# Optimization experiments

Measured on AMD Instinct MI355X. Metric: run time of the kernel, lower is better.

Reference implementation:

```python
import jax, jax.numpy as jnp
import numpy as np

N_NODES = 500_000
N_EDGES = 16_000_000
N_LAYERS = 49
ALPHA = 0.3  # GCN2Conv alpha; beta = 1.0 (no theta/layer given)

# per-layer activation applied AFTER the conv (layer index 0-based)
_LEAKY = {1, 11, 21, 31, 41}
_SIG = {4, 14, 24, 34, 44}


def setup_inputs() -> dict:
    key = jax.random.key(0)
    k1, k2, k3 = jax.random.split(key, 3)
    x = jax.random.normal(k1, (N_NODES, 1), dtype=jnp.float32)
    adj = jax.random.randint(k2, (2, N_EDGES), 0, N_NODES, dtype=jnp.int64)
    # 49 scalar (1x1) layer weights
    w = jax.random.normal(k3, (N_LAYERS,), dtype=jnp.float32) * 0.1
    return {"input": x, "w": w, "adj": adj}


def _gcn_norm(adj, n):
    # add self-loops, symmetric normalization D^-1/2 (A+I) D^-1/2
    loops = jnp.arange(n, dtype=adj.dtype)
    src = jnp.concatenate([adj[0], loops])
    dst = jnp.concatenate([adj[1], loops])
    deg = jax.ops.segment_sum(jnp.ones(src.shape[0], jnp.float32), dst, num_segments=n)
    dis = 1.0 / jnp.sqrt(deg)  # deg >= 1 due to self-loops
    ew = dis[src] * dis[dst]
    return src, dst, ew


def reference(input, w, adj):
    n = input.shape[0]
    x0 = input.astype(jnp.float32)
    src, dst, ew = _gcn_norm(adj, n)
    ewc = ew[:, None]  # [E+N, 1]

    def gcn2(x, wl):
        h = jax.ops.segment_sum(ewc * x[src], dst, num_segments=n)  # A_hat @ x
        comb = (1.0 - ALPHA) * h + ALPHA * x0                       # residual mix
        return comb * wl                                            # 1x1 weight, beta=1

    x = x0
    for i in range(N_LAYERS):
        y = gcn2(x, w[i])
        if i == 0:
            x = y  # no activation after gcn1
        elif i == N_LAYERS - 1:
            x = n * jax.nn.sigmoid(y)  # CustomSigmoid: len(x) * sigmoid(x)
        elif i in _LEAKY:
            x = jax.nn.leaky_relu(y, 0.01)
        elif i in _SIG:
            x = jax.nn.sigmoid(y)
        else:
            x = jax.nn.relu(y)
        # dropout(p=0.0) is identity
    return jnp.squeeze(x, 1).astype(jnp.int64)
```

## Files before the change

kernel.cpp:

```cpp
#include <hip/hip_runtime.h>
#include <math.h>

#define NN 500000
#define NE 16000000
#define BSH 9
#define NBKT 977
#define PB2 65536
#define NPB2 ((NE + PB2 - 1) / PB2)
#define BKT_CAP 17920

__global__ __launch_bounds__(1024) void hist_kernel(const int4* __restrict__ dst4,
                                                    int* __restrict__ bcnt) {
    __shared__ int lh[NBKT];
    for (int i = threadIdx.x; i < NBKT; i += 1024) lh[i] = 0;
    __syncthreads();
    long base4 = (long)blockIdx.x * (PB2 / 4);
    for (int k = 0; k < PB2 / 4; k += 1024) {
        long i4 = base4 + k + threadIdx.x;
        if (i4 < NE / 4) {
            int4 d = dst4[i4];
            atomicAdd(&lh[d.x >> BSH], 1);
            atomicAdd(&lh[d.y >> BSH], 1);
            atomicAdd(&lh[d.z >> BSH], 1);
            atomicAdd(&lh[d.w >> BSH], 1);
        }
    }
    __syncthreads();
    for (int i = threadIdx.x; i < NBKT; i += 1024) {
        int c = lh[i];
        if (c) atomicAdd(&bcnt[i], c);
    }
}

__global__ __launch_bounds__(256) void scan_buckets(int* __restrict__ bcnt,
                                                    int* __restrict__ bbase) {
    __shared__ int sh[256];
    __shared__ int carry_sh;
    if (threadIdx.x == 0) carry_sh = 0;
    __syncthreads();
    for (int base = 0; base < NBKT; base += 256) {
        int i = base + threadIdx.x;
        int v = (i < NBKT) ? bcnt[i] : 0;
        sh[threadIdx.x] = v;
        __syncthreads();
        for (int off = 1; off < 256; off <<= 1) {
            int t = (threadIdx.x >= off) ? sh[threadIdx.x - off] : 0;
            __syncthreads();
            sh[threadIdx.x] += t;
            __syncthreads();
        }
        int incl = sh[threadIdx.x];
        int c = carry_sh;
        __syncthreads();
        if (i < NBKT) {
            int ex = c + incl - v;
            bbase[i] = ex;
            bcnt[i] = ex;
        }
        if (threadIdx.x == 255) carry_sh = c + incl;
        __syncthreads();
    }
    if (threadIdx.x == 0) bbase[NBKT] = NE;
}

__global__ __launch_bounds__(1024) void partition_kernel(const int4* __restrict__ src4,
                                                         const int4* __restrict__ dst4,
                                                         int* __restrict__ bcur,
                                                         int* __restrict__ ebuf) {
    __shared__ int lh[NBKT];
    for (int i = threadIdx.x; i < NBKT; i += 1024) lh[i] = 0;
    __syncthreads();
    long base4 = (long)blockIdx.x * (PB2 / 4);
    for (int k = 0; k < PB2 / 4; k += 1024) {
        long i4 = base4 + k + threadIdx.x;
        if (i4 < NE / 4) {
            int4 d = dst4[i4];
            atomicAdd(&lh[d.x >> BSH], 1);
            atomicAdd(&lh[d.y >> BSH], 1);
            atomicAdd(&lh[d.z >> BSH], 1);
            atomicAdd(&lh[d.w >> BSH], 1);
        }
    }
    __syncthreads();
    for (int i = threadIdx.x; i < NBKT; i += 1024) {
        int c = lh[i];
        if (c) lh[i] = atomicAdd(&bcur[i], c);
    }
    __syncthreads();
    for (int k = 0; k < PB2 / 4; k += 1024) {
        long i4 = base4 + k + threadIdx.x;
        if (i4 < NE / 4) {
            int4 d = dst4[i4];
            int4 s = src4[i4];
            int pos;
            pos = atomicAdd(&lh[d.x >> BSH], 1); ebuf[pos] = ((d.x & 511) << 19) | s.x;
            pos = atomicAdd(&lh[d.y >> BSH], 1); ebuf[pos] = ((d.y & 511) << 19) | s.y;
            pos = atomicAdd(&lh[d.z >> BSH], 1); ebuf[pos] = ((d.z & 511) << 19) | s.z;
            pos = atomicAdd(&lh[d.w >> BSH], 1); ebuf[pos] = ((d.w & 511) << 19) | s.w;
        }
    }
}

__global__ __launch_bounds__(512) void bucket_csr(const int* __restrict__ bbase,
                                                  int* __restrict__ ebuf,
                                                  int* __restrict__ rp,
                                                  float* __restrict__ dis,
                                                  const float* __restrict__ x0,
                                                  float* __restrict__ z0) {
    __shared__ int eds[BKT_CAP];
    __shared__ int outb[BKT_CAP];
    __shared__ int cnt[512];
    __shared__ int scn[512];
    int b = blockIdx.x;
    int ebase = bbase[b];
    int nb = bbase[b + 1] - ebase;
    if (nb > BKT_CAP) nb = BKT_CAP;
    for (int i = threadIdx.x; i < nb; i += 512) eds[i] = ebuf[ebase + i];
    cnt[threadIdx.x] = 0;
    __syncthreads();
    for (int i = threadIdx.x; i < nb; i += 512) atomicAdd(&cnt[eds[i] >> 19], 1);
    __syncthreads();
    int my = cnt[threadIdx.x];
    scn[threadIdx.x] = my;
    __syncthreads();
    for (int off = 1; off < 512; off <<= 1) {
        int t = (threadIdx.x >= off) ? scn[threadIdx.x - off] : 0;
        __syncthreads();
        scn[threadIdx.x] += t;
        __syncthreads();
    }
    int excl = scn[threadIdx.x] - my;
    int v = b * 512 + threadIdx.x;
    if (v < NN) {
        rp[v] = ebase + excl;
        float dv = rsqrtf((float)(my + 1));
        dis[v] = dv;
        z0[v] = x0[v] * dv;
    }
    __syncthreads();
    cnt[threadIdx.x] = excl;
    __syncthreads();
    for (int i = threadIdx.x; i < nb; i += 512) {
        int p = eds[i];
        int pos = atomicAdd(&cnt[p >> 19], 1);
        outb[pos] = p & 0x7FFFF;
    }
    __syncthreads();
    for (int i = threadIdx.x; i < nb; i += 512) ebuf[ebase + i] = outb[i];
    if (b == 0 && threadIdx.x == 0) rp[NN] = NE;
}

__global__ __launch_bounds__(256) void layer_kernel(
        const int* __restrict__ rp, const int* __restrict__ csr,
        const float* __restrict__ zin, const float* __restrict__ dis,
        const float* __restrict__ x0, const float* __restrict__ w,
        int li, int act, float* __restrict__ zout, int* __restrict__ out) {
    int tid = blockIdx.x * 256 + threadIdx.x;
    int v = tid >> 3;
    int lane = threadIdx.x & 7;
    int beg = rp[v];
    int end = rp[v + 1];
    float s = 0.f;
    int j = beg + lane;
    for (; j + 24 < end; j += 32) {
        int c0 = csr[j];
        int c1 = csr[j + 8];
        int c2 = csr[j + 16];
        int c3 = csr[j + 24];
        float z0 = __hip_atomic_load(&zin[c0], __ATOMIC_RELAXED, __HIP_MEMORY_SCOPE_AGENT);
        float z1 = __hip_atomic_load(&zin[c1], __ATOMIC_RELAXED, __HIP_MEMORY_SCOPE_AGENT);
        float z2 = __hip_atomic_load(&zin[c2], __ATOMIC_RELAXED, __HIP_MEMORY_SCOPE_AGENT);
        float z3 = __hip_atomic_load(&zin[c3], __ATOMIC_RELAXED, __HIP_MEMORY_SCOPE_AGENT);
        s += z0; s += z1; s += z2; s += z3;
    }
    for (; j < end; j += 8)
        s += __hip_atomic_load(&zin[csr[j]], __ATOMIC_RELAXED, __HIP_MEMORY_SCOPE_AGENT);
    s += __shfl_xor(s, 1);
    s += __shfl_xor(s, 2);
    s += __shfl_xor(s, 4);
    if (lane != 0) return;
    s += zin[v];
    float h = dis[v] * s;
    float comb = 0.7f * h + 0.3f * x0[v];
    float y = comb * w[li];
    if (act == 4) {
        float sg = 1.f / (1.f + expf(-y));
        out[v] = (int)(500000.f * sg);
        return;
    }
    float r;
    if (act == 0)      r = y;
    else if (act == 1) r = fmaxf(y, 0.f);
    else if (act == 2) r = (y > 0.f) ? y : 0.01f * y;
    else               r = 1.f / (1.f + expf(-y));
    zout[v] = dis[v] * r;
}

extern "C" void kernel_launch(void* const* d_in, const int* in_sizes, int n_in,
                              void* d_out, int out_size, void* d_ws, size_t ws_size,
                              hipStream_t stream) {
    const float* x0  = (const float*)d_in[0];
    const float* w   = (const float*)d_in[1];
    const int*   adj = (const int*)d_in[2];
    const int*   src = adj;
    const int*   dst = adj + NE;
    int* out = (int*)d_out;

    uintptr_t p = (uintptr_t)d_ws;
    auto alloc = [&](size_t bytes) -> void* {
        p = (p + 255) & ~(uintptr_t)255;
        void* r = (void*)p;
        p += bytes;
        return r;
    };
    float* dis   = (float*)alloc((size_t)NN * 4);
    int*   rp    = (int*)alloc((size_t)(NN + 1) * 4);
    float* z0    = (float*)alloc((size_t)NN * 4);
    float* z1    = (float*)alloc((size_t)NN * 4);
    int*   bcnt  = (int*)alloc((size_t)NBKT * 4);
    int*   bbase = (int*)alloc((size_t)(NBKT + 1) * 4);
    int*   csr   = (int*)alloc((size_t)NE * 4);
    (void)ws_size;

    hipMemsetAsync(bcnt, 0, (size_t)NBKT * 4, stream);

    hist_kernel<<<NPB2, 1024, 0, stream>>>((const int4*)dst, bcnt);
    scan_buckets<<<1, 256, 0, stream>>>(bcnt, bbase);
    partition_kernel<<<NPB2, 1024, 0, stream>>>((const int4*)src, (const int4*)dst, bcnt, csr);
    bucket_csr<<<NBKT, 512, 0, stream>>>(bbase, csr, rp, dis, x0, z0);

    float* zbuf[2] = {z0, z1};
    const int LB = (NN * 8) / 256;
    for (int i = 0; i < 49; i++) {
        int act;
        if (i == 0)            act = 0;
        else if (i == 48)      act = 4;
        else if (i % 10 == 1)  act = 2;
        else if (i % 10 == 4)  act = 3;
        else                   act = 1;
        layer_kernel<<<LB, 256, 0, stream>>>(rp, csr, zbuf[i & 1], dis, x0, w,
                                             i, act, zbuf[(i + 1) & 1], out);
    }
}
```

Baseline: 4.054 ms.

## Replace CSR pull SpMV with 2D-tiled shared-memory scatter and combine pass

```diff
diff --git a/kernel.cpp b/kernel.cpp
--- a/kernel.cpp
+++ b/kernel.cpp
@@ -1,199 +1,244 @@
 #include <hip/hip_runtime.h>
 #include <math.h>
+#include <stdint.h>
 
 #define NN 500000
 #define NE 16000000
-#define BSH 9
-#define NBKT 977
-#define PB2 65536
-#define NPB2 ((NE + PB2 - 1) / PB2)
-#define BKT_CAP 17920
-
-__global__ __launch_bounds__(1024) void hist_kernel(const int4* __restrict__ dst4,
+#define NT 62
+#define NQ 8
+#define OCTW 62500
+#define NCH (NT * NQ)
+#define PB 65536
+#define NPB ((NE + PB - 1) / PB)
+#define CH_CAP 34000
+#define ZPAD 524288
+#define SENT 0xFFFFFFFFu
+
+__global__ __launch_bounds__(1024) void hist_kernel(const int4* __restrict__ src4,
+                                                    const int4* __restrict__ dst4,
                                                     int* __restrict__ bcnt) {
-    __shared__ int lh[NBKT];
-    for (int i = threadIdx.x; i < NBKT; i += 1024) lh[i] = 0;
-    __syncthreads();
-    long base4 = (long)blockIdx.x * (PB2 / 4);
-    for (int k = 0; k < PB2 / 4; k += 1024) {
+    __shared__ int lh[NCH];
+    for (int i = threadIdx.x; i < NCH; i += 1024) lh[i] = 0;
+    __syncthreads();
+    long base4 = (long)blockIdx.x * (PB / 4);
+    for (int k = 0; k < PB / 4; k += 1024) {
         long i4 = base4 + k + threadIdx.x;
         if (i4 < NE / 4) {
             int4 d = dst4[i4];
-            atomicAdd(&lh[d.x >> BSH], 1);
-            atomicAdd(&lh[d.y >> BSH], 1);
-            atomicAdd(&lh[d.z >> BSH], 1);
-            atomicAdd(&lh[d.w >> BSH], 1);
+            int4 s = src4[i4];
+            atomicAdd(&lh[(d.x >> 13) * NQ + s.x / OCTW], 1);
+            atomicAdd(&lh[(d.y >> 13) * NQ + s.y / OCTW], 1);
+            atomicAdd(&lh[(d.z >> 13) * NQ + s.z / OCTW], 1);
+            atomicAdd(&lh[(d.w >> 13) * NQ + s.w / OCTW], 1);
         }
     }
     __syncthreads();
-    for (int i = threadIdx.x; i < NBKT; i += 1024) {
+    for (int i = threadIdx.x; i < NCH; i += 1024) {
         int c = lh[i];
         if (c) atomicAdd(&bcnt[i], c);
     }
 }
 
-__global__ __launch_bounds__(256) void scan_buckets(int* __restrict__ bcnt,
-                                                    int* __restrict__ bbase) {
-    __shared__ int sh[256];
-    __shared__ int carry_sh;
-    if (threadIdx.x == 0) carry_sh = 0;
-    __syncthreads();
-    for (int base = 0; base < NBKT; base += 256) {
-        int i = base + threadIdx.x;
-        int v = (i < NBKT) ? bcnt[i] : 0;
-        sh[threadIdx.x] = v;
-        __syncthreads();
-        for (int off = 1; off < 256; off <<= 1) {
-            int t = (threadIdx.x >= off) ? sh[threadIdx.x - off] : 0;
-            __syncthreads();
-            sh[threadIdx.x] += t;
-            __syncthreads();
-        }
-        int incl = sh[threadIdx.x];
-        int c = carry_sh;
-        __syncthreads();
-        if (i < NBKT) {
-            int ex = c + incl - v;
-            bbase[i] = ex;
-            bcnt[i] = ex;
-        }
-        if (threadIdx.x == 255) carry_sh = c + incl;
-        __syncthreads();
-    }
-    if (threadIdx.x == 0) bbase[NBKT] = NE;
+__global__ __launch_bounds__(512) void scan_buckets(const int* __restrict__ bcnt,
+                                                    int* __restrict__ bbase,
+                                                    int* __restrict__ bcur) {
+    __shared__ int scn[512];
+    __shared__ int tot;
+    int i = threadIdx.x;
+    int v = (i < NCH) ? bcnt[i] : 0;
+    int pv = (v + 15) & ~15;
+    scn[i] = pv;
+    __syncthreads();
+    for (int off = 1; off < 512; off <<= 1) {
+        int t = (i >= off) ? scn[i - off] : 0;
+        __syncthreads();
+        scn[i] += t;
+        __syncthreads();
+    }
+    int excl = scn[i] - pv;
+    if (i < NCH) { bbase[i] = excl; bcur[i] = excl; }
+    if (i == 511) tot = scn[511];
+    __syncthreads();
+    if (i == 0) bbase[NCH] = tot;
 }
 
 __global__ __launch_bounds__(1024) void partition_kernel(const int4* __restrict__ src4,
                                                          const int4* __restrict__ dst4,
                                                          int* __restrict__ bcur,
-                                                         int* __restrict__ ebuf) {
-    __shared__ int lh[NBKT];
-    for (int i = threadIdx.x; i < NBKT; i += 1024) lh[i] = 0;
-    __syncthreads();
-    long base4 = (long)blockIdx.x * (PB2 / 4);
-    for (int k = 0; k < PB2 / 4; k += 1024) {
+                                                         uint32_t* __restrict__ ebuf) {
+    __shared__ int lh[NCH];
+    for (int i = threadIdx.x; i < NCH; i += 1024) lh[i] = 0;
+    __syncthreads();
+    long base4 = (long)blockIdx.x * (PB / 4);
+    for (int k = 0; k < PB / 4; k += 1024) {
         long i4 = base4 + k + threadIdx.x;
         if (i4 < NE / 4) {
             int4 d = dst4[i4];
-            atomicAdd(&lh[d.x >> BSH], 1);
-            atomicAdd(&lh[d.y >> BSH], 1);
-            atomicAdd(&lh[d.z >> BSH], 1);
-            atomicAdd(&lh[d.w >> BSH], 1);
+            int4 s = src4[i4];
+            atomicAdd(&lh[(d.x >> 13) * NQ + s.x / OCTW], 1);
+            atomicAdd(&lh[(d.y >> 13) * NQ + s.y / OCTW], 1);
+            atomicAdd(&lh[(d.z >> 13) * NQ + s.z / OCTW], 1);
+            atomicAdd(&lh[(d.w >> 13) * NQ + s.w / OCTW], 1);
         }
     }
     __syncthreads();
-    for (int i = threadIdx.x; i < NBKT; i += 1024) {
+    for (int i = threadIdx.x; i < NCH; i += 1024) {
         int c = lh[i];
         if (c) lh[i] = atomicAdd(&bcur[i], c);
     }
     __syncthreads();
-    for (int k = 0; k < PB2 / 4; k += 1024) {
+    for (int k = 0; k < PB / 4; k += 1024) {
         long i4 = base4 + k + threadIdx.x;
         if (i4 < NE / 4) {
             int4 d = dst4[i4];
             int4 s = src4[i4];
             int pos;
-            pos = atomicAdd(&lh[d.x >> BSH], 1); ebuf[pos] = ((d.x & 511) << 19) | s.x;
-            pos = atomicAdd(&lh[d.y >> BSH], 1); ebuf[pos] = ((d.y & 511) << 19) | s.y;
-            pos = atomicAdd(&lh[d.z >> BSH], 1); ebuf[pos] = ((d.z & 511) << 19) | s.z;
-            pos = atomicAdd(&lh[d.w >> BSH], 1); ebuf[pos] = ((d.w & 511) << 19) | s.w;
+            pos = atomicAdd(&lh[(d.x >> 13) * NQ + s.x / OCTW], 1);
+            ebuf[pos] = ((uint32_t)(d.x & 8191) << 19) | (uint32_t)s.x;
+            pos = atomicAdd(&lh[(d.y >> 13) * NQ + s.y / OCTW], 1);
+            ebuf[pos] = ((uint32_t)(d.y & 8191) << 19) | (uint32_t)s.y;
+            pos = atomicAdd(&lh[(d.z >> 13) * NQ + s.z / OCTW], 1);
+            ebuf[pos] = ((uint32_t)(d.z & 8191) << 19) | (uint32_t)s.z;
+            pos = atomicAdd(&lh[(d.w >> 13) * NQ + s.w / OCTW], 1);
+            ebuf[pos] = ((uint32_t)(d.w & 8191) << 19) | (uint32_t)s.w;
         }
     }
 }
 
-__global__ __launch_bounds__(512) void bucket_csr(const int* __restrict__ bbase,
-                                                  int* __restrict__ ebuf,
-                                                  int* __restrict__ rp,
-                                                  float* __restrict__ dis,
-                                                  const float* __restrict__ x0,
-                                                  float* __restrict__ z0) {
-    __shared__ int eds[BKT_CAP];
-    __shared__ int outb[BKT_CAP];
-    __shared__ int cnt[512];
-    __shared__ int scn[512];
-    int b = blockIdx.x;
-    int ebase = bbase[b];
-    int nb = bbase[b + 1] - ebase;
-    if (nb > BKT_CAP) nb = BKT_CAP;
-    for (int i = threadIdx.x; i < nb; i += 512) eds[i] = ebuf[ebase + i];
-    cnt[threadIdx.x] = 0;
-    __syncthreads();
-    for (int i = threadIdx.x; i < nb; i += 512) atomicAdd(&cnt[eds[i] >> 19], 1);
-    __syncthreads();
-    int my = cnt[threadIdx.x];
-    scn[threadIdx.x] = my;
-    __syncthreads();
-    for (int off = 1; off < 512; off <<= 1) {
-        int t = (threadIdx.x >= off) ? scn[threadIdx.x - off] : 0;
-        __syncthreads();
-        scn[threadIdx.x] += t;
-        __syncthreads();
-    }
-    int excl = scn[threadIdx.x] - my;
-    int v = b * 512 + threadIdx.x;
+__global__ __launch_bounds__(1024) void chunk_sort(const int* __restrict__ bcnt,
+                                                   const int* __restrict__ bbase,
+                                                   uint32_t* __restrict__ ebuf,
+                                                   int* __restrict__ deg) {
+    __shared__ uint32_t sorted[CH_CAP];
+    __shared__ int ghist[4096];
+    __shared__ int scn[1024];
+    int c = blockIdx.x;
+    int base = bbase[c];
+    int pend = bbase[c + 1];
+    int n = bcnt[c];
+    if (n > CH_CAP) n = CH_CAP;
+    int t = c >> 3;
+    int octbase = (c & 7) * OCTW;
+    int* dh = (int*)sorted;
+    for (int i = threadIdx.x; i < 4096; i += 1024) ghist[i] = 0;
+    for (int i = threadIdx.x; i < 8192; i += 1024) dh[i] = 0;
+    __syncthreads();
+    for (int i = threadIdx.x; i < n; i += 1024) {
+        uint32_t w = ebuf[base + i];
+        int s = (int)(w & 0x7FFFFu);
+        atomicAdd(&ghist[(s - octbase) >> 4], 1);
+        atomicAdd(&dh[w >> 19], 1);
+    }
+    __syncthreads();
+    for (int i = threadIdx.x; i < 8192; i += 1024) {
+        int d = dh[i];
+        if (d) atomicAdd(&deg[t * 8192 + i], d);
+    }
+    __syncthreads();
+    int b4 = threadIdx.x * 4;
+    int l0 = ghist[b4], l1 = ghist[b4 + 1], l2 = ghist[b4 + 2], l3 = ghist[b4 + 3];
+    int ls = l0 + l1 + l2 + l3;
+    scn[threadIdx.x] = ls;
+    __syncthreads();
+    for (int off = 1; off < 1024; off <<= 1) {
+        int tv = (threadIdx.x >= off) ? scn[threadIdx.x - off] : 0;
+        __syncthreads();
+        scn[threadIdx.x] += tv;
+        __syncthreads();
+    }
+    int ex = scn[threadIdx.x] - ls;
+    ghist[b4] = ex; ghist[b4 + 1] = ex + l0;
+    ghist[b4 + 2] = ex + l0 + l1; ghist[b4 + 3] = ex + l0 + l1 + l2;
+    __syncthreads();
+    for (int i = threadIdx.x; i < n; i += 1024) {
+        uint32_t w = ebuf[base + i];
+        int k = ((int)(w & 0x7FFFFu) - octbase) >> 4;
+        int pos = atomicAdd(&ghist[k], 1);
+        sorted[pos] = w;
+    }
+    __syncthreads();
+    for (int i = threadIdx.x; base + i < pend; i += 1024)
+        ebuf[base + i] = (i < n) ? sorted[i] : SENT;
+}
+
+__global__ void dis_kernel(const int* __restrict__ deg, const float* __restrict__ x0,
+                           float* __restrict__ dis, float* __restrict__ z0) {
+    int v = blockIdx.x * 512 + threadIdx.x;
     if (v < NN) {
-        rp[v] = ebase + excl;
-        float dv = rsqrtf((float)(my + 1));
-        dis[v] = dv;
-        z0[v] = x0[v] * dv;
-    }
-    __syncthreads();
-    cnt[threadIdx.x] = excl;
-    __syncthreads();
-    for (int i = threadIdx.x; i < nb; i += 512) {
-        int p = eds[i];
-        int pos = atomicAdd(&cnt[p >> 19], 1);
-        outb[pos] = p & 0x7FFFF;
-    }
-    __syncthreads();
-    for (int i = threadIdx.x; i < nb; i += 512) ebuf[ebase + i] = outb[i];
-    if (b == 0 && threadIdx.x == 0) rp[NN] = NE;
-}
-
-__global__ __launch_bounds__(256) void layer_kernel(
-        const int* __restrict__ rp, const int* __restrict__ csr,
-        const float* __restrict__ zin, const float* __restrict__ dis,
-        const float* __restrict__ x0, const float* __restrict__ w,
-        int li, int act, float* __restrict__ zout, int* __restrict__ out) {
-    int tid = blockIdx.x * 256 + threadIdx.x;
-    int v = tid >> 3;
-    int lane = threadIdx.x & 7;
-    int beg = rp[v];
-    int end = rp[v + 1];
-    float s = 0.f;
-    int j = beg + lane;
-    for (; j + 24 < end; j += 32) {
-        int c0 = csr[j];
-        int c1 = csr[j + 8];
-        int c2 = csr[j + 16];
-        int c3 = csr[j + 24];
-        float z0 = __hip_atomic_load(&zin[c0], __ATOMIC_RELAXED, __HIP_MEMORY_SCOPE_AGENT);
-        float z1 = __hip_atomic_load(&zin[c1], __ATOMIC_RELAXED, __HIP_MEMORY_SCOPE_AGENT);
-        float z2 = __hip_atomic_load(&zin[c2], __ATOMIC_RELAXED, __HIP_MEMORY_SCOPE_AGENT);
-        float z3 = __hip_atomic_load(&zin[c3], __ATOMIC_RELAXED, __HIP_MEMORY_SCOPE_AGENT);
-        s += z0; s += z1; s += z2; s += z3;
-    }
-    for (; j < end; j += 8)
-        s += __hip_atomic_load(&zin[csr[j]], __ATOMIC_RELAXED, __HIP_MEMORY_SCOPE_AGENT);
-    s += __shfl_xor(s, 1);
-    s += __shfl_xor(s, 2);
-    s += __shfl_xor(s, 4);
-    if (lane != 0) return;
-    s += zin[v];
-    float h = dis[v] * s;
-    float comb = 0.7f * h + 0.3f * x0[v];
-    float y = comb * w[li];
+        float d = rsqrtf((float)(deg[v] + 1));
+        dis[v] = d;
+        z0[v] = x0[v] * d;
+    }
+}
+
+__global__ __launch_bounds__(1024) void scatter_kernel(const int* __restrict__ bbase,
+                                                       const uint32_t* __restrict__ ebuf,
+                                                       const float* __restrict__ zin,
+                                                       float* __restrict__ hp) {
+    __shared__ float acc[8192];
+    int c = blockIdx.x;
+    for (int i = threadIdx.x; i < 8192; i += 1024) acc[i] = 0.f;
+    __syncthreads();
+    int b4 = bbase[c] >> 2, e4 = bbase[c + 1] >> 2;
+    const uint4* __restrict__ eb4 = (const uint4*)ebuf;
+    for (int i4 = b4 + threadIdx.x; i4 < e4; i4 += 1024) {
+        uint4 w = eb4[i4];
+        float a0 = zin[w.x & 0x7FFFFu];
+        float a1 = zin[w.y & 0x7FFFFu];
+        float a2 = zin[w.z & 0x7FFFFu];
+        float a3 = zin[w.w & 0x7FFFFu];
+        atomicAdd(&acc[w.x >> 19], a0);
+        atomicAdd(&acc[w.y >> 19], a1);
+        atomicAdd(&acc[w.z >> 19], a2);
+        atomicAdd(&acc[w.w >> 19], a3);
+    }
+    __syncthreads();
+    int t = c >> 3, q = c & 7;
+    float* dstp = hp + (size_t)q * (NT * 8192) + t * 8192;
+    for (int k = threadIdx.x; k < 8192; k += 1024) dstp[k] = acc[k];
+}
+
+__global__ __launch_bounds__(512) void combine_kernel(const float4* __restrict__ hp4,
+        const float4* __restrict__ zin4, const float4* __restrict__ dis4,
+        const float4* __restrict__ x04, const float* __restrict__ w,
+        int li, int act, float4* __restrict__ zout4, int4* __restrict__ out4) {
+    int v4 = blockIdx.x * 512 + threadIdx.x;
+    if (v4 >= NN / 4) return;
+    float4 s = zin4[v4];
+    #pragma unroll
+    for (int q = 0; q < NQ; q++) {
+        float4 hq = hp4[(size_t)q * (NT * 8192 / 4) + v4];
+        s.x += hq.x; s.y += hq.y; s.z += hq.z; s.w += hq.w;
+    }
+    float4 dv = dis4[v4];
+    float4 xv = x04[v4];
+    float wl = w[li];
+    float y0 = (0.7f * dv.x * s.x + 0.3f * xv.x) * wl;
+    float y1 = (0.7f * dv.y * s.y + 0.3f * xv.y) * wl;
+    float y2 = (0.7f * dv.z * s.z + 0.3f * xv.z) * wl;
+    float y3 = (0.7f * dv.w * s.w + 0.3f * xv.w) * wl;
     if (act == 4) {
-        float sg = 1.f / (1.f + expf(-y));
-        out[v] = (int)(500000.f * sg);
+        int4 o;
+        o.x = (int)(500000.f / (1.f + expf(-y0)));
+        o.y = (int)(500000.f / (1.f + expf(-y1)));
+        o.z = (int)(500000.f / (1.f + expf(-y2)));
+        o.w = (int)(500000.f / (1.f + expf(-y3)));
+        out4[v4] = o;
         return;
     }
-    float r;
-    if (act == 0)      r = y;
-    else if (act == 1) r = fmaxf(y, 0.f);
-    else if (act == 2) r = (y > 0.f) ? y : 0.01f * y;
-    else               r = 1.f / (1.f + expf(-y));
-    zout[v] = dis[v] * r;
+    float r0, r1, r2, r3;
+    if (act == 0)      { r0 = y0; r1 = y1; r2 = y2; r3 = y3; }
+    else if (act == 1) { r0 = fmaxf(y0, 0.f); r1 = fmaxf(y1, 0.f);
+                         r2 = fmaxf(y2, 0.f); r3 = fmaxf(y3, 0.f); }
+    else if (act == 2) { r0 = (y0 > 0.f) ? y0 : 0.01f * y0;
+                         r1 = (y1 > 0.f) ? y1 : 0.01f * y1;
+                         r2 = (y2 > 0.f) ? y2 : 0.01f * y2;
+                         r3 = (y3 > 0.f) ? y3 : 0.01f * y3; }
+    else               { r0 = 1.f / (1.f + expf(-y0)); r1 = 1.f / (1.f + expf(-y1));
+                         r2 = 1.f / (1.f + expf(-y2)); r3 = 1.f / (1.f + expf(-y3)); }
+    float4 zo;
+    zo.x = dv.x * r0; zo.y = dv.y * r1; zo.z = dv.z * r2; zo.w = dv.w * r3;
+    zout4[v4] = zo;
 }
 
 extern "C" void kernel_launch(void* const* d_in, const int* in_sizes, int n_in,
@@ -214,23 +259,29 @@
         return r;
     };
     float* dis   = (float*)alloc((size_t)NN * 4);
-    int*   rp    = (int*)alloc((size_t)(NN + 1) * 4);
-    float* z0    = (float*)alloc((size_t)NN * 4);
-    float* z1    = (float*)alloc((size_t)NN * 4);
-    int*   bcnt  = (int*)alloc((size_t)NBKT * 4);
-    int*   bbase = (int*)alloc((size_t)(NBKT + 1) * 4);
-    int*   csr   = (int*)alloc((size_t)NE * 4);
+    float* z0    = (float*)alloc((size_t)ZPAD * 4);
+    float* z1    = (float*)alloc((size_t)ZPAD * 4);
+    int*   bcnt  = (int*)alloc((size_t)NCH * 4);
+    int*   bbase = (int*)alloc((size_t)(NCH + 1) * 4);
+    int*   bcur  = (int*)alloc((size_t)NCH * 4);
+    uint32_t* csr = (uint32_t*)alloc(((size_t)NE + 8192) * 4);
+    float* hp    = (float*)alloc((size_t)NQ * NT * 8192 * 4);
+    int*   deg   = (int*)hp;
     (void)ws_size;
 
-    hipMemsetAsync(bcnt, 0, (size_t)NBKT * 4, stream);
-
-    hist_kernel<<<NPB2, 1024, 0, stream>>>((const int4*)dst, bcnt);
-    scan_buckets<<<1, 256, 0, stream>>>(bcnt, bbase);
-    partition_kernel<<<NPB2, 1024, 0, stream>>>((const int4*)src, (const int4*)dst, bcnt, csr);
-    bucket_csr<<<NBKT, 512, 0, stream>>>(bbase, csr, rp, dis, x0, z0);
+    hipMemsetAsync(bcnt, 0, (size_t)NCH * 4, stream);
+    hipMemsetAsync(deg, 0, (size_t)NT * 8192 * 4, stream);
+    hipMemsetAsync(z0, 0, (size_t)ZPAD * 4, stream);
+    hipMemsetAsync(z1, 0, (size_t)ZPAD * 4, stream);
+
+    hist_kernel<<<NPB, 1024, 0, stream>>>((const int4*)src, (const int4*)dst, bcnt);
+    scan_buckets<<<1, 512, 0, stream>>>(bcnt, bbase, bcur);
+    partition_kernel<<<NPB, 1024, 0, stream>>>((const int4*)src, (const int4*)dst, bcur, csr);
+    chunk_sort<<<NCH, 1024, 0, stream>>>(bcnt, bbase, csr, deg);
+    dis_kernel<<<(NN + 511) / 512, 512, 0, stream>>>(deg, x0, dis, z0);
 
     float* zbuf[2] = {z0, z1};
-    const int LB = (NN * 8) / 256;
+    const int CB = (NN / 4 + 511) / 512;
     for (int i = 0; i < 49; i++) {
         int act;
         if (i == 0)            act = 0;
@@ -238,7 +289,9 @@
         else if (i % 10 == 1)  act = 2;
         else if (i % 10 == 4)  act = 3;
         else                   act = 1;
-        layer_kernel<<<LB, 256, 0, stream>>>(rp, csr, zbuf[i & 1], dis, x0, w,
-                                             i, act, zbuf[(i + 1) & 1], out);
-    }
-}
+        scatter_kernel<<<NCH, 1024, 0, stream>>>(bbase, csr, zbuf[i & 1], hp);
+        combine_kernel<<<CB, 512, 0, stream>>>((const float4*)hp, (const float4*)zbuf[i & 1],
+                                               (const float4*)dis, (const float4*)x0, w,
+                                               i, act, (float4*)zbuf[(i + 1) & 1], (int4*)out);
+    }
+}
```

Measured after the change: 4.935 ms. 21.7% more time.

## Partition edges into fixed-capacity bucket slots and use nontemporal CSR loads

Applied to the files above, without the earlier changes.

```diff
diff --git a/kernel.cpp b/kernel.cpp
--- a/kernel.cpp
+++ b/kernel.cpp
@@ -3,107 +3,58 @@
 
 #define NN 500000
 #define NE 16000000
-#define BSH 9
 #define NBKT 977
-#define PB2 65536
-#define NPB2 ((NE + PB2 - 1) / PB2)
+#define PB 65536
+#define NPB ((NE + PB - 1) / PB)
 #define BKT_CAP 17920
+#define SLOTB 17920
 
-__global__ __launch_bounds__(1024) void hist_kernel(const int4* __restrict__ dst4,
-                                                    int* __restrict__ bcnt) {
+__global__ __launch_bounds__(1024) void partition_kernel(const int4* __restrict__ src4,
+                                                         const int4* __restrict__ dst4,
+                                                         int* __restrict__ bcnt,
+                                                         int* __restrict__ ebuf) {
     __shared__ int lh[NBKT];
     for (int i = threadIdx.x; i < NBKT; i += 1024) lh[i] = 0;
     __syncthreads();
-    long base4 = (long)blockIdx.x * (PB2 / 4);
-    for (int k = 0; k < PB2 / 4; k += 1024) {
+    long base4 = (long)blockIdx.x * (PB / 4);
+    for (int k = 0; k < PB / 4; k += 1024) {
         long i4 = base4 + k + threadIdx.x;
         if (i4 < NE / 4) {
             int4 d = dst4[i4];
-            atomicAdd(&lh[d.x >> BSH], 1);
-            atomicAdd(&lh[d.y >> BSH], 1);
-            atomicAdd(&lh[d.z >> BSH], 1);
-            atomicAdd(&lh[d.w >> BSH], 1);
+            atomicAdd(&lh[d.x >> 9], 1);
+            atomicAdd(&lh[d.y >> 9], 1);
+            atomicAdd(&lh[d.z >> 9], 1);
+            atomicAdd(&lh[d.w >> 9], 1);
         }
     }
     __syncthreads();
     for (int i = threadIdx.x; i < NBKT; i += 1024) {
         int c = lh[i];
-        if (c) atomicAdd(&bcnt[i], c);
-    }
-}
-
-__global__ __launch_bounds__(256) void scan_buckets(int* __restrict__ bcnt,
-                                                    int* __restrict__ bbase) {
-    __shared__ int sh[256];
-    __shared__ int carry_sh;
-    if (threadIdx.x == 0) carry_sh = 0;
-    __syncthreads();
-    for (int base = 0; base < NBKT; base += 256) {
-        int i = base + threadIdx.x;
-        int v = (i < NBKT) ? bcnt[i] : 0;
-        sh[threadIdx.x] = v;
-        __syncthreads();
-        for (int off = 1; off < 256; off <<= 1) {
-            int t = (threadIdx.x >= off) ? sh[threadIdx.x - off] : 0;
-            __syncthreads();
-            sh[threadIdx.x] += t;
-            __syncthreads();
-        }
-        int incl = sh[threadIdx.x];
-        int c = carry_sh;
-        __syncthreads();
-        if (i < NBKT) {
-            int ex = c + incl - v;
-            bbase[i] = ex;
-            bcnt[i] = ex;
-        }
-        if (threadIdx.x == 255) carry_sh = c + incl;
-        __syncthreads();
-    }
-    if (threadIdx.x == 0) bbase[NBKT] = NE;
-}
-
-__global__ __launch_bounds__(1024) void partition_kernel(const int4* __restrict__ src4,
-                                                         const int4* __restrict__ dst4,
-                                                         int* __restrict__ bcur,
-                                                         int* __restrict__ ebuf) {
-    __shared__ int lh[NBKT];
-    for (int i = threadIdx.x; i < NBKT; i += 1024) lh[i] = 0;
-    __syncthreads();
-    long base4 = (long)blockIdx.x * (PB2 / 4);
-    for (int k = 0; k < PB2 / 4; k += 1024) {
-        long i4 = base4 + k + threadIdx.x;
-        if (i4 < NE / 4) {
-            int4 d = dst4[i4];
-            atomicAdd(&lh[d.x >> BSH], 1);
-            atomicAdd(&lh[d.y >> BSH], 1);
-            atomicAdd(&lh[d.z >> BSH], 1);
-            atomicAdd(&lh[d.w >> BSH], 1);
-        }
+        if (c) lh[i] = atomicAdd(&bcnt[i], c);
     }
     __syncthreads();
-    for (int i = threadIdx.x; i < NBKT; i += 1024) {
-        int c = lh[i];
-        if (c) lh[i] = atomicAdd(&bcur[i], c);
-    }
-    __syncthreads();
-    for (int k = 0; k < PB2 / 4; k += 1024) {
+    for (int k = 0; k < PB / 4; k += 1024) {
         long i4 = base4 + k + threadIdx.x;
         if (i4 < NE / 4) {
             int4 d = dst4[i4];
             int4 s = src4[i4];
-            int pos;
-            pos = atomicAdd(&lh[d.x >> BSH], 1); ebuf[pos] = ((d.x & 511) << 19) | s.x;
-            pos = atomicAdd(&lh[d.y >> BSH], 1); ebuf[pos] = ((d.y & 511) << 19) | s.y;
-            pos = atomicAdd(&lh[d.z >> BSH], 1); ebuf[pos] = ((d.z & 511) << 19) | s.z;
-            pos = atomicAdd(&lh[d.w >> BSH], 1); ebuf[pos] = ((d.w & 511) << 19) | s.w;
+            int b, rel;
+            b = d.x >> 9; rel = atomicAdd(&lh[b], 1);
+            if (rel < SLOTB) ebuf[(long)b * SLOTB + rel] = ((d.x & 511) << 19) | s.x;
+            b = d.y >> 9; rel = atomicAdd(&lh[b], 1);
+            if (rel < SLOTB) ebuf[(long)b * SLOTB + rel] = ((d.y & 511) << 19) | s.y;
+            b = d.z >> 9; rel = atomicAdd(&lh[b], 1);
+            if (rel < SLOTB) ebuf[(long)b * SLOTB + rel] = ((d.z & 511) << 19) | s.z;
+            b = d.w >> 9; rel = atomicAdd(&lh[b], 1);
+            if (rel < SLOTB) ebuf[(long)b * SLOTB + rel] = ((d.w & 511) << 19) | s.w;
         }
     }
 }
 
-__global__ __launch_bounds__(512) void bucket_csr(const int* __restrict__ bbase,
+__global__ __launch_bounds__(512) void bucket_csr(const int* __restrict__ bcnt,
                                                   int* __restrict__ ebuf,
                                                   int* __restrict__ rp,
+                                                  int* __restrict__ re,
                                                   float* __restrict__ dis,
                                                   const float* __restrict__ x0,
                                                   float* __restrict__ z0) {
@@ -112,8 +63,8 @@
     __shared__ int cnt[512];
     __shared__ int scn[512];
     int b = blockIdx.x;
-    int ebase = bbase[b];
-    int nb = bbase[b + 1] - ebase;
+    long ebase = (long)b * SLOTB;
+    int nb = bcnt[b];
     if (nb > BKT_CAP) nb = BKT_CAP;
     for (int i = threadIdx.x; i < nb; i += 512) eds[i] = ebuf[ebase + i];
     cnt[threadIdx.x] = 0;
@@ -132,7 +83,8 @@
     int excl = scn[threadIdx.x] - my;
     int v = b * 512 + threadIdx.x;
     if (v < NN) {
-        rp[v] = ebase + excl;
+        rp[v] = (int)ebase + excl;
+        re[v] = (int)ebase + excl + my;
         float dv = rsqrtf((float)(my + 1));
         dis[v] = dv;
         z0[v] = x0[v] * dv;
@@ -147,11 +99,11 @@
     }
     __syncthreads();
     for (int i = threadIdx.x; i < nb; i += 512) ebuf[ebase + i] = outb[i];
-    if (b == 0 && threadIdx.x == 0) rp[NN] = NE;
 }
 
 __global__ __launch_bounds__(256) void layer_kernel(
-        const int* __restrict__ rp, const int* __restrict__ csr,
+        const int* __restrict__ rp, const int* __restrict__ re,
+        const int* __restrict__ csr,
         const float* __restrict__ zin, const float* __restrict__ dis,
         const float* __restrict__ x0, const float* __restrict__ w,
         int li, int act, float* __restrict__ zout, int* __restrict__ out) {
@@ -159,22 +111,21 @@
     int v = tid >> 3;
     int lane = threadIdx.x & 7;
     int beg = rp[v];
-    int end = rp[v + 1];
+    int end = re[v];
     float s = 0.f;
     int j = beg + lane;
     for (; j + 24 < end; j += 32) {
-        int c0 = csr[j];
-        int c1 = csr[j + 8];
-        int c2 = csr[j + 16];
-        int c3 = csr[j + 24];
-        float z0 = __hip_atomic_load(&zin[c0], __ATOMIC_RELAXED, __HIP_MEMORY_SCOPE_AGENT);
-        float z1 = __hip_atomic_load(&zin[c1], __ATOMIC_RELAXED, __HIP_MEMORY_SCOPE_AGENT);
-        float z2 = __hip_atomic_load(&zin[c2], __ATOMIC_RELAXED, __HIP_MEMORY_SCOPE_AGENT);
-        float z3 = __hip_atomic_load(&zin[c3], __ATOMIC_RELAXED, __HIP_MEMORY_SCOPE_AGENT);
+        int c0 = __builtin_nontemporal_load(csr + j);
+        int c1 = __builtin_nontemporal_load(csr + j + 8);
+        int c2 = __builtin_nontemporal_load(csr + j + 16);
+        int c3 = __builtin_nontemporal_load(csr + j + 24);
+        float z0 = zin[c0];
+        float z1 = zin[c1];
+        float z2 = zin[c2];
+        float z3 = zin[c3];
         s += z0; s += z1; s += z2; s += z3;
     }
-    for (; j < end; j += 8)
-        s += __hip_atomic_load(&zin[csr[j]], __ATOMIC_RELAXED, __HIP_MEMORY_SCOPE_AGENT);
+    for (; j < end; j += 8) s += zin[__builtin_nontemporal_load(csr + j)];
     s += __shfl_xor(s, 1);
     s += __shfl_xor(s, 2);
     s += __shfl_xor(s, 4);
@@ -213,21 +164,19 @@
         p += bytes;
         return r;
     };
-    float* dis   = (float*)alloc((size_t)NN * 4);
-    int*   rp    = (int*)alloc((size_t)(NN + 1) * 4);
-    float* z0    = (float*)alloc((size_t)NN * 4);
-    float* z1    = (float*)alloc((size_t)NN * 4);
-    int*   bcnt  = (int*)alloc((size_t)NBKT * 4);
-    int*   bbase = (int*)alloc((size_t)(NBKT + 1) * 4);
-    int*   csr   = (int*)alloc((size_t)NE * 4);
+    float* dis  = (float*)alloc((size_t)NN * 4);
+    int*   rp   = (int*)alloc((size_t)NN * 4);
+    int*   re   = (int*)alloc((size_t)NN * 4);
+    float* z0   = (float*)alloc((size_t)NN * 4);
+    float* z1   = (float*)alloc((size_t)NN * 4);
+    int*   bcnt = (int*)alloc((size_t)NBKT * 4);
+    int*   csr  = (int*)alloc((size_t)NBKT * SLOTB * 4);
     (void)ws_size;
 
     hipMemsetAsync(bcnt, 0, (size_t)NBKT * 4, stream);
 
-    hist_kernel<<<NPB2, 1024, 0, stream>>>((const int4*)dst, bcnt);
-    scan_buckets<<<1, 256, 0, stream>>>(bcnt, bbase);
-    partition_kernel<<<NPB2, 1024, 0, stream>>>((const int4*)src, (const int4*)dst, bcnt, csr);
-    bucket_csr<<<NBKT, 512, 0, stream>>>(bbase, csr, rp, dis, x0, z0);
+    partition_kernel<<<NPB, 1024, 0, stream>>>((const int4*)src, (const int4*)dst, bcnt, csr);
+    bucket_csr<<<NBKT, 512, 0, stream>>>(bcnt, csr, rp, re, dis, x0, z0);
 
     float* zbuf[2] = {z0, z1};
     const int LB = (NN * 8) / 256;
@@ -238,7 +187,7 @@
         else if (i % 10 == 1)  act = 2;
         else if (i % 10 == 4)  act = 3;
         else                   act = 1;
-        layer_kernel<<<LB, 256, 0, stream>>>(rp, csr, zbuf[i & 1], dis, x0, w,
+        layer_kernel<<<LB, 256, 0, stream>>>(rp, re, csr, zbuf[i & 1], dis, x0, w,
                                              i, act, zbuf[(i + 1) & 1], out);
     }
 }
```

New measurement: 5.576 ms. +37.5%, slower.
